# Kernel optimization log

Measured on AMD Instinct MI355X. Metric: run time of the kernel, lower is better.

## Reference

```python
import jax, jax.numpy as jnp
import numpy as np

B, T, S, G, D, H, W, CHUNK = 2, 4096, 4096, 64, 1024, 16, 512, 256
HD = D // H


def setup_inputs() -> dict:
    key = jax.random.key(0)
    ks = jax.random.split(key, 16)
    std = 1.0 / np.sqrt(D)
    w = lambda k: jax.random.normal(k, (D, D), jnp.float32) * std
    b = lambda k: jax.random.normal(k, (D,), jnp.float32) * 0.01
    return {
        "query": jax.random.normal(ks[0], (B, T, D), jnp.float32),
        "encoder_out": jax.random.normal(ks[1], (B, S, D), jnp.float32),
        "global_tokens": jax.random.normal(ks[2], (B, G, D), jnp.float32),
        "qw": w(ks[3]), "qb": b(ks[4]),
        "kw": w(ks[5]), "kb": b(ks[6]),
        "vw": w(ks[7]), "vb": b(ks[8]),
        "gkw": w(ks[9]), "gkb": b(ks[10]),
        "gvw": w(ks[11]), "gvb": b(ks[12]),
        "ow": w(ks[13]), "ob": b(ks[14]),
        "compression_ratio": 1,
    }


def reference(query, encoder_out, global_tokens, qw, qb, kw, kb, vw, vb,
              gkw, gkb, gvw, gvb, ow, ob, compression_ratio):
    scale = jnp.float32(np.sqrt(HD))
    r = jnp.float32(compression_ratio)
    # expected raw position for each decoder step, clamped to valid src range
    expected = jnp.clip((jnp.arange(T, dtype=jnp.float32) / r).astype(jnp.int32), 0, S - 1)
    expected = jnp.broadcast_to(expected[None], (B, T))  # [B,T]

    lin = lambda x, wt, bs: x @ wt.T + bs  # torch nn.Linear: y = x W^T + b
    q = lin(query, qw, qb).reshape(B, T, H, HD).transpose(0, 2, 1, 3)            # [B,H,T,HD]
    gk = lin(global_tokens, gkw, gkb).reshape(B, G, H, HD).transpose(0, 2, 1, 3)  # [B,H,G,HD]
    gv = lin(global_tokens, gvw, gvb).reshape(B, G, H, HD).transpose(0, 2, 1, 3)
    ak = lin(encoder_out, kw, kb).reshape(B, S, H, HD).transpose(0, 2, 1, 3)      # [B,H,S,HD]
    av = lin(encoder_out, vw, vb).reshape(B, S, H, HD).transpose(0, 2, 1, 3)

    nC = T // CHUNK
    # per-(batch,chunk) window start, from the middle query's expected position
    centers = expected.reshape(B, nC, CHUNK)[:, :, CHUNK // 2]   # [B,nC]
    win_start = jnp.clip(centers - W // 2, 0, S - W)             # [B,nC]; window always full length W
    idx = win_start[:, :, None] + jnp.arange(W)[None, None, :]   # [B,nC,W]

    gather = lambda kv_b, idx_b: kv_b[:, idx_b, :]               # [H,S,HD],[nC,W] -> [H,nC,W,HD]
    wk = jax.vmap(gather)(ak, idx)                               # [B,H,nC,W,HD]
    wv = jax.vmap(gather)(av, idx)

    qc = q.reshape(B, H, nC, CHUNK, HD)
    sg = jnp.einsum('bhcqd,bhgd->bhcqg', qc, gk) / scale          # global scores  [B,H,nC,CHUNK,G]
    sl = jnp.einsum('bhcqd,bhcwd->bhcqw', qc, wk) / scale         # windowed scores [B,H,nC,CHUNK,W]
    attn = jax.nn.softmax(jnp.concatenate([sg, sl], axis=-1), axis=-1)
    out = (jnp.einsum('bhcqg,bhgd->bhcqd', attn[..., :G], gv)
           + jnp.einsum('bhcqw,bhcwd->bhcqd', attn[..., G:], wv))  # [B,H,nC,CHUNK,HD]
    out = out.reshape(B, H, T, HD).transpose(0, 2, 1, 3).reshape(B, T, D)
    return lin(out, ow, ob)
```

## Files before the change

### kernel.cpp

```cpp
#include <hip/hip_runtime.h>

typedef unsigned short u16;
typedef unsigned int u32;
typedef __attribute__((ext_vector_type(4))) float f32x4;
typedef __attribute__((ext_vector_type(16))) float f32x16;
typedef __attribute__((ext_vector_type(8))) short bf16x8;

constexpr int B_ = 2, T_ = 4096, S_ = 4096, G_ = 64, D_ = 1024, H_ = 16, W_ = 512, CHUNK_ = 256;
constexpr int NC_ = T_ / CHUNK_;
constexpr int NT_ = (G_ + W_) / 32;

__device__ __forceinline__ u16 f2bf(float x) {
  u32 u = __builtin_bit_cast(u32, x);
  return (u16)((u + 0x7FFFu + ((u >> 16) & 1u)) >> 16);
}

__global__ __launch_bounds__(256) void cvt_all_kernel(const float* __restrict__ q, const float* __restrict__ e,
                                                      const float* __restrict__ g, const float* __restrict__ w0,
                                                      const float* __restrict__ w1, const float* __restrict__ w2,
                                                      const float* __restrict__ w3, const float* __restrict__ w4,
                                                      const float* __restrict__ w5, u16* __restrict__ dst) {
  int blk = blockIdx.x;
  const float* src;
  int sblk;
  if (blk < 8192) { src = q; sblk = 0; }
  else if (blk < 16384) { src = e; sblk = 8192; }
  else if (blk < 16512) { src = g; sblk = 16384; }
  else if (blk < 17536) { src = w0; sblk = 16512; }
  else if (blk < 18560) { src = w1; sblk = 17536; }
  else if (blk < 19584) { src = w2; sblk = 18560; }
  else if (blk < 20608) { src = w3; sblk = 19584; }
  else if (blk < 21632) { src = w4; sblk = 20608; }
  else { src = w5; sblk = 21632; }
  int li = (blk - sblk) * 256 + threadIdx.x;
  size_t gi = (size_t)blk * 256 + threadIdx.x;
  float4 v = ((const float4*)src)[li];
  uint2 o;
  o.x = (u32)f2bf(v.x) | ((u32)f2bf(v.y) << 16);
  o.y = (u32)f2bf(v.z) | ((u32)f2bf(v.w) << 16);
  ((uint2*)dst)[gi] = o;
}

template <int MODE>
__global__ __launch_bounds__(256) void gemm_kernel(const u16* __restrict__ A, const u16* __restrict__ Bt,
                                                   const float* __restrict__ bias, const float* __restrict__ bias2,
                                                   size_t split, void* __restrict__ out) {
  __shared__ char lds[32768];
  char* As = lds;
  char* Bs = lds + 16384;
  const int tid = threadIdx.x;
  const int lane = tid & 63;
  const int wv = tid >> 6;
  const int wr = wv >> 1, wc = wv & 1;
  const int l15 = lane & 15, kg = lane >> 4;
  const int row0 = blockIdx.x * 128;
  const int col0 = blockIdx.y * 128;

  f32x4 acc[4][4];
#pragma unroll
  for (int i = 0; i < 4; i++)
#pragma unroll
    for (int j = 0; j < 4; j++)
#pragma unroll
      for (int r = 0; r < 4; r++) acc[i][j][r] = 0.f;

  const char* Abase = (const char*)A;
  const char* Bbase = (const char*)Bt;

  const int kb = 16 * ((lane & 3) ^ ((lane >> 3) & 3));
  auto stage = [&](int bufsel, int k0) {
#pragma unroll
    for (int c = 0; c < 2; c++) {
      int arow = wv * 32 + c * 16 + (lane >> 2);
      int dsto = bufsel * 8192 + wv * 2048 + c * 1024 + lane * 16;
      const char* ga = Abase + ((size_t)(row0 + arow) * 2048 + (size_t)k0 * 2 + kb);
      __builtin_amdgcn_global_load_lds((const __attribute__((address_space(1))) void*)ga,
                                       (__attribute__((address_space(3))) void*)(As + dsto), 16, 0, 0);
      const char* gb = Bbase + ((size_t)(col0 + arow) * 2048 + (size_t)k0 * 2 + kb);
      __builtin_amdgcn_global_load_lds((const __attribute__((address_space(1))) void*)gb,
                                       (__attribute__((address_space(3))) void*)(Bs + dsto), 16, 0, 0);
    }
  };

  stage(0, 0);
  __syncthreads();

  for (int it = 0; it < 32; ++it) {
    const int cur = it & 1;
    if (it + 1 < 32) stage(cur ^ 1, (it + 1) * 32);

    const char* Ab = As + cur * 8192;
    const char* Bb = Bs + cur * 8192;
    bf16x8 af[4], bfv[4];
#pragma unroll
    for (int mi = 0; mi < 4; mi++) {
      int row = wr * 64 + mi * 16 + l15;
      af[mi] = *(const bf16x8*)(Ab + ((row * 64 + kg * 16) ^ ((row & 6) << 3)));
    }
#pragma unroll
    for (int ni = 0; ni < 4; ni++) {
      int row = wc * 64 + ni * 16 + l15;
      bfv[ni] = *(const bf16x8*)(Bb + ((row * 64 + kg * 16) ^ ((row & 6) << 3)));
    }
    __builtin_amdgcn_s_setprio(1);
#pragma unroll
    for (int mi = 0; mi < 4; mi++)
#pragma unroll
      for (int ni = 0; ni < 4; ni++)
        acc[mi][ni] = __builtin_amdgcn_mfma_f32_16x16x32_bf16(bfv[ni], af[mi], acc[mi][ni], 0, 0, 0);
    __builtin_amdgcn_s_setprio(0);
    __syncthreads();
  }

  const float* bp = bias;
  size_t obase = 0;
  if (MODE == 3 && col0 >= 1024) {
    bp = bias2 - 1024;
    obase = split - 1024;
  }
  float4 bv4[4];
#pragma unroll
  for (int ni = 0; ni < 4; ni++) bv4[ni] = *(const float4*)&bp[col0 + wc * 64 + ni * 16 + kg * 4];
#pragma unroll
  for (int mi = 0; mi < 4; mi++) {
    size_t grow = (size_t)(row0 + wr * 64 + mi * 16 + l15);
#pragma unroll
    for (int ni = 0; ni < 4; ni++) {
      int gcol = col0 + wc * 64 + ni * 16 + kg * 4;
      float v0 = acc[mi][ni][0] + bv4[ni].x;
      float v1 = acc[mi][ni][1] + bv4[ni].y;
      float v2 = acc[mi][ni][2] + bv4[ni].z;
      float v3 = acc[mi][ni][3] + bv4[ni].w;
      if (MODE == 1) {
        v0 *= 0.18033688011112042f; v1 *= 0.18033688011112042f;
        v2 *= 0.18033688011112042f; v3 *= 0.18033688011112042f;
      }
      if (MODE == 2) {
        float4 fo = {v0, v1, v2, v3};
        *(float4*)&((float*)out)[grow * 1024 + gcol] = fo;
      } else {
        uint2 o;
        asm("v_cvt_pk_bf16_f32 %0, %1, %2" : "=v"(o.x) : "v"(v0), "v"(v1));
        asm("v_cvt_pk_bf16_f32 %0, %1, %2" : "=v"(o.y) : "v"(v2), "v"(v3));
        *(uint2*)&((u16*)out)[obase + grow * 1024 + gcol] = o;
      }
    }
  }
}

__global__ __launch_bounds__(512, 4) void attn_kernel(const u16* __restrict__ q_bf, const u16* __restrict__ k_bf,
                                                      const u16* __restrict__ v_bf, const u16* __restrict__ gk_bf,
                                                      const u16* __restrict__ gv_bf, u16* __restrict__ ao,
                                                      const int* __restrict__ rptr) {
  __shared__ u16 smem[16384];
  const int c = blockIdx.x, h = blockIdx.y, b = blockIdx.z;
  const int tid = threadIdx.x;
  const int lane = tid & 63, wv = tid >> 6;
  const int l31 = lane & 31, half = lane >> 5;
  const int t0 = c * CHUNK_;

  int rr = rptr[0];
  int centert = c * CHUNK_ + CHUNK_ / 2;
  int expected = (int)((float)centert / (float)rr);
  expected = min(max(expected, 0), S_ - 1);
  int ws0 = min(max(expected - W_ / 2, 0), S_ - W_);

  bf16x8 qf[4];
  {
    const u16* qrow = q_bf + ((size_t)(b * T_ + t0 + wv * 32 + l31)) * D_ + h * 64 + half * 8;
#pragma unroll
    for (int s = 0; s < 4; s++) qf[s] = *(const bf16x8*)(qrow + s * 16);
  }

  const int skey = (tid & 255) >> 3, shq = tid & 7;
  const bool isK = tid < 256;

  auto load_tile = [&](int j) -> uint4 {
    const u16* base;
    size_t row;
    if (j < 2) {
      base = isK ? gk_bf : gv_bf;
      row = (size_t)(b * G_ + j * 32 + skey);
    } else {
      base = isK ? k_bf : v_bf;
      row = (size_t)(b * S_ + ws0 + (j - 2) * 32 + skey);
    }
    return *(const uint4*)(base + row * D_ + h * 64 + shq * 8);
  };

  f32x16 oacc[2];
#pragma unroll
  for (int i = 0; i < 2; i++)
#pragma unroll
    for (int r = 0; r < 16; r++) oacc[i][r] = 0.f;
  float mrun = -1e30f, lsum = 0.f;

  uint4 stg = load_tile(0);

  for (int j = 0; j < NT_; j++) {
    const int bsel = j & 1;
    if (isK) {
      *(uint4*)((char*)smem + bsel * 4096 + ((skey * 128 + shq * 16) ^ ((skey & 7) << 4))) = stg;
    } else {
      const u16* pv = (const u16*)&stg;
      char* bp = (char*)smem + 8192 + bsel * 5248 + shq * 656 + skey * 2;
#pragma unroll
      for (int e = 0; e < 8; e++) *(u16*)(bp + e * 80) = pv[e];
    }
    if (j + 1 < NT_) stg = load_tile(j + 1);
    __syncthreads();

    const int kbase = bsel * 4096;
    const int vtb = 8192 + bsel * 5248;

    f32x16 sacc;
#pragma unroll
    for (int r = 0; r < 16; r++) sacc[r] = 0.f;
    __builtin_amdgcn_s_setprio(1);
#pragma unroll
    for (int s = 0; s < 4; s++) {
      int kb = kbase + ((l31 * 128 + half * 16 + s * 32) ^ ((l31 & 7) << 4));
      bf16x8 kf = *(const bf16x8*)((char*)smem + kb);
      sacc = __builtin_amdgcn_mfma_f32_32x32x16_bf16(kf, qf[s], sacc, 0, 0, 0);
    }
    __builtin_amdgcn_s_setprio(0);

    float t0m = fmaxf(fmaxf(sacc[0], sacc[1]), sacc[2]);
    float t1m = fmaxf(fmaxf(sacc[3], sacc[4]), sacc[5]);
    float t2m = fmaxf(fmaxf(sacc[6], sacc[7]), sacc[8]);
    float t3m = fmaxf(fmaxf(sacc[9], sacc[10]), sacc[11]);
    float t4m = fmaxf(fmaxf(sacc[12], sacc[13]), sacc[14]);
    float tmax = fmaxf(fmaxf(fmaxf(t0m, t1m), fmaxf(t2m, t3m)), fmaxf(t4m, sacc[15]));
    tmax = fmaxf(tmax, __shfl_xor(tmax, 32));
    if (__any(tmax > mrun + 8.f)) {
      float mnew = fmaxf(mrun, tmax);
      float fac = __builtin_amdgcn_exp2f(mrun - mnew);
      mrun = mnew;
      lsum *= fac;
#pragma unroll
      for (int i = 0; i < 2; i++)
#pragma unroll
        for (int r = 0; r < 16; r++) oacc[i][r] *= fac;
    }
    float p[16];
#pragma unroll
    for (int r = 0; r < 16; r++) p[r] = __builtin_amdgcn_exp2f(sacc[r] - mrun);
    float s0s = (p[0] + p[1]) + (p[2] + p[3]);
    float s1s = (p[4] + p[5]) + (p[6] + p[7]);
    float s2s = (p[8] + p[9]) + (p[10] + p[11]);
    float s3s = (p[12] + p[13]) + (p[14] + p[15]);
    float tsum = (s0s + s1s) + (s2s + s3s);
    tsum += __shfl_xor(tsum, 32);
    lsum += tsum;

    u32 xs[8], px[8];
#pragma unroll
    for (int i = 0; i < 8; i++)
      asm("v_cvt_pk_bf16_f32 %0, %1, %2" : "=v"(xs[i]) : "v"(p[2 * i]), "v"(p[2 * i + 1]));
#pragma unroll
    for (int i = 0; i < 8; i++) px[i] = (u32)__shfl_xor((int)xs[i], 32);
    u32 Bk[2][4];
    Bk[0][0] = half ? px[2] : xs[0];
    Bk[0][1] = half ? px[3] : xs[1];
    Bk[0][2] = half ? xs[2] : px[0];
    Bk[0][3] = half ? xs[3] : px[1];
    Bk[1][0] = half ? px[6] : xs[4];
    Bk[1][1] = half ? px[7] : xs[5];
    Bk[1][2] = half ? xs[6] : px[4];
    Bk[1][3] = half ? xs[7] : px[5];

    int vro = vtb + l31 * 80 + ((l31 >> 3) << 4) + half * 16;
    __builtin_amdgcn_s_setprio(1);
#pragma unroll
    for (int hdf = 0; hdf < 2; hdf++) {
#pragma unroll
      for (int ks = 0; ks < 2; ks++) {
        bf16x8 vf = *(const bf16x8*)((const char*)smem + vro + hdf * 2624 + ks * 32);
        uint4 u4;
        u4.x = Bk[ks][0]; u4.y = Bk[ks][1]; u4.z = Bk[ks][2]; u4.w = Bk[ks][3];
        bf16x8 pb = __builtin_bit_cast(bf16x8, u4);
        oacc[hdf] = __builtin_amdgcn_mfma_f32_32x32x16_bf16(vf, pb, oacc[hdf], 0, 0, 0);
      }
    }
    __builtin_amdgcn_s_setprio(0);
  }

  __syncthreads();
  float inv = 1.f / lsum;
#pragma unroll
  for (int hdf = 0; hdf < 2; hdf++) {
#pragma unroll
    for (int a = 0; a < 4; a++) {
      float f0 = oacc[hdf][4 * a] * inv, f1 = oacc[hdf][4 * a + 1] * inv;
      float f2 = oacc[hdf][4 * a + 2] * inv, f3 = oacc[hdf][4 * a + 3] * inv;
      uint2 o;
      asm("v_cvt_pk_bf16_f32 %0, %1, %2" : "=v"(o.x) : "v"(f0), "v"(f1));
      asm("v_cvt_pk_bf16_f32 %0, %1, %2" : "=v"(o.y) : "v"(f2), "v"(f3));
      int off = wv * 4096 + l31 * 128 + ((16 * a + 8 * half + 64 * hdf) ^ ((l31 & 7) << 4));
      *(uint2*)((char*)smem + off) = o;
    }
  }
  __syncthreads();
#pragma unroll
  for (int it = 0; it < 4; it++) {
    int byteo = (tid + it * 512) * 16;
    int row = byteo >> 7;
    int colb = byteo & 127;
    uint4 vv = *(const uint4*)((const char*)smem + row * 128 + (colb ^ ((row & 7) << 4)));
    *(uint4*)(ao + ((size_t)(b * T_ + t0 + row)) * D_ + h * 64 + (colb >> 1)) = vv;
  }
}

extern "C" void kernel_launch(void* const* d_in, const int* in_sizes, int n_in,
                              void* d_out, int out_size, void* d_ws, size_t ws_size,
                              hipStream_t stream) {
  (void)in_sizes; (void)n_in; (void)out_size; (void)ws_size;
  const float* query = (const float*)d_in[0];
  const float* enc = (const float*)d_in[1];
  const float* glob = (const float*)d_in[2];
  const float* qw = (const float*)d_in[3];
  const float* qb = (const float*)d_in[4];
  const float* kw = (const float*)d_in[5];
  const float* kb = (const float*)d_in[6];
  const float* vw = (const float*)d_in[7];
  const float* vb = (const float*)d_in[8];
  const float* gkw = (const float*)d_in[9];
  const float* gkb = (const float*)d_in[10];
  const float* gvw = (const float*)d_in[11];
  const float* gvb = (const float*)d_in[12];
  const float* ow = (const float*)d_in[13];
  const float* ob = (const float*)d_in[14];
  const int* rp = (const int*)d_in[15];

  const size_t NQ = (size_t)B_ * T_ * D_;
  const size_t NG = (size_t)B_ * G_ * D_;
  const size_t NW = (size_t)D_ * D_;

  u16* ws = (u16*)d_ws;
  u16* qx = ws;
  u16* ex = qx + NQ;
  u16* gx = ex + NQ;
  u16* wgt = gx + NG;
  u16* q_bf = wgt + 6 * NW;
  u16* k_bf = q_bf + NQ;
  u16* v_bf = k_bf + NQ;
  u16* gk_bf = v_bf + NQ;
  u16* gv_bf = gk_bf + NG;
  u16* ao = gv_bf + NG;

  cvt_all_kernel<<<22656, 256, 0, stream>>>(query, enc, glob, qw, kw, vw, gkw, gvw, ow, ws);

  gemm_kernel<1><<<dim3(64, 8), 256, 0, stream>>>(qx, wgt + 0 * NW, qb, qb, 0, q_bf);
  gemm_kernel<3><<<dim3(64, 16), 256, 0, stream>>>(ex, wgt + 1 * NW, kb, vb, NQ, k_bf);
  gemm_kernel<3><<<dim3(1, 16), 256, 0, stream>>>(gx, wgt + 3 * NW, gkb, gvb, NG, gk_bf);

  attn_kernel<<<dim3(NC_, H_, B_), 512, 0, stream>>>(q_bf, k_bf, v_bf, gk_bf, gv_bf, ao, rp);

  gemm_kernel<2><<<dim3(64, 8), 256, 0, stream>>>(ao, wgt + 5 * NW, ob, ob, 0, d_out);
}
```

Measured before the change: 171.2 us.

## Use 256x256-tile triple-buffered GEMM kernel for fused K/V projection

Adds a new GEMM kernel that uses 256x256 output tiles with 512 threads. It stages tiles straight from global memory into LDS with global_load_lds, triple-buffers them, uses a swizzled LDS layout, and interleaves loads with MFMA phases. The fused K/V projection of encoder_out now uses this kernel instead of the generic one, aiming for more operand reuse per tile and better overlap of loads with compute. The grid becomes 256 blocks of 512 threads, which may fill the GPU's compute units less evenly, and the large 96 KB LDS footprint limits occupancy.

```diff
diff --git a/kernel.cpp b/kernel.cpp
--- a/kernel.cpp
+++ b/kernel.cpp
@@ -148,6 +148,136 @@
   }
 }
 
+template <int MODE>
+__global__ __launch_bounds__(512, 2) void gemm256_kernel(const u16* __restrict__ A, const u16* __restrict__ Bt,
+                                                         const float* __restrict__ bias, const float* __restrict__ bias2,
+                                                         size_t split, void* __restrict__ out) {
+  __shared__ char lds[98304];
+  const int tid = threadIdx.x;
+  const int lane = tid & 63;
+  const int wid = tid >> 6;
+  const int wm = wid >> 2, wn = wid & 3;
+  const int l15 = lane & 15, kg = lane >> 4;
+  const int bid = blockIdx.x;
+  const int swz = (bid & 7) * 32 + (bid >> 3);
+  const int row0 = (swz & 31) * 256;
+  const int col0 = (swz >> 5) * 256;
+
+  f32x4 acc[8][4];
+#pragma unroll
+  for (int i = 0; i < 8; i++)
+#pragma unroll
+    for (int j = 0; j < 4; j++)
+#pragma unroll
+      for (int r = 0; r < 4; r++) acc[i][j][r] = 0.f;
+
+  const char* Abase = (const char*)A;
+  const char* Bbase = (const char*)Bt;
+  const int kb = 16 * ((tid & 3) ^ ((tid >> 3) & 3));
+  const int rl0 = tid >> 2;
+
+  auto stageOp = [&](const char* base, int rowbase, int ldsbase, int kt) {
+#pragma unroll
+    for (int j = 0; j < 2; j++) {
+      int dst = ldsbase + tid * 16 + j * 8192;
+      const char* g = base + (size_t)(rowbase + rl0 + j * 128) * 2048 + kt * 64 + kb;
+      __builtin_amdgcn_global_load_lds((const __attribute__((address_space(1))) void*)g,
+                                       (__attribute__((address_space(3))) void*)(lds + dst), 16, 0, 0);
+    }
+  };
+
+  stageOp(Abase, row0, 0, 0);
+  stageOp(Bbase, col0, 49152, 0);
+  stageOp(Abase, row0, 16384, 1);
+  stageOp(Bbase, col0, 49152 + 16384, 1);
+  asm volatile("s_waitcnt vmcnt(4)" ::: "memory");
+  __builtin_amdgcn_s_barrier();
+
+  int cur = 0, nx = 2;
+  for (int t = 0; t < 32; ++t) {
+    const char* Ab = lds + cur * 16384;
+    const char* Bb = lds + 49152 + cur * 16384;
+    bf16x8 bfv[4], af[4];
+#pragma unroll
+    for (int ni = 0; ni < 4; ni++) {
+      int r = wn * 64 + ni * 16 + l15;
+      bfv[ni] = *(const bf16x8*)(Bb + ((r * 64 + kg * 16) ^ (((r >> 1) & 3) << 4)));
+    }
+#pragma unroll
+    for (int mi = 0; mi < 4; mi++) {
+      int r = wm * 128 + mi * 16 + l15;
+      af[mi] = *(const bf16x8*)(Ab + ((r * 64 + kg * 16) ^ (((r >> 1) & 3) << 4)));
+    }
+    if (t + 2 < 32) stageOp(Abase, row0, nx * 16384, t + 2);
+    __builtin_amdgcn_s_barrier();
+    __builtin_amdgcn_s_setprio(1);
+#pragma unroll
+    for (int mi = 0; mi < 4; mi++)
+#pragma unroll
+      for (int ni = 0; ni < 4; ni++)
+        acc[mi][ni] = __builtin_amdgcn_mfma_f32_16x16x32_bf16(bfv[ni], af[mi], acc[mi][ni], 0, 0, 0);
+    __builtin_amdgcn_s_setprio(0);
+    __builtin_amdgcn_s_barrier();
+#pragma unroll
+    for (int mi = 0; mi < 4; mi++) {
+      int r = wm * 128 + (mi + 4) * 16 + l15;
+      af[mi] = *(const bf16x8*)(Ab + ((r * 64 + kg * 16) ^ (((r >> 1) & 3) << 4)));
+    }
+    if (t + 2 < 32) stageOp(Bbase, col0, 49152 + nx * 16384, t + 2);
+    __builtin_amdgcn_s_barrier();
+    __builtin_amdgcn_s_setprio(1);
+#pragma unroll
+    for (int mi = 0; mi < 4; mi++)
+#pragma unroll
+      for (int ni = 0; ni < 4; ni++)
+        acc[mi + 4][ni] = __builtin_amdgcn_mfma_f32_16x16x32_bf16(bfv[ni], af[mi], acc[mi + 4][ni], 0, 0, 0);
+    __builtin_amdgcn_s_setprio(0);
+    if (t < 30) {
+      asm volatile("s_waitcnt vmcnt(4)" ::: "memory");
+    } else if (t == 30) {
+      asm volatile("s_waitcnt vmcnt(0)" ::: "memory");
+    }
+    __builtin_amdgcn_s_barrier();
+    cur = cur == 2 ? 0 : cur + 1;
+    nx = nx == 2 ? 0 : nx + 1;
+  }
+
+  const float* bp = bias;
+  size_t obase = 0;
+  if (MODE == 3 && col0 >= 1024) {
+    bp = bias2 - 1024;
+    obase = split - 1024;
+  }
+  float4 bv4[4];
+#pragma unroll
+  for (int ni = 0; ni < 4; ni++) bv4[ni] = *(const float4*)&bp[col0 + wn * 64 + ni * 16 + kg * 4];
+#pragma unroll
+  for (int mi = 0; mi < 8; mi++) {
+    size_t grow = (size_t)(row0 + wm * 128 + mi * 16 + l15);
+#pragma unroll
+    for (int ni = 0; ni < 4; ni++) {
+      int gcol = col0 + wn * 64 + ni * 16 + kg * 4;
+      float v0 = acc[mi][ni][0] + bv4[ni].x;
+      float v1 = acc[mi][ni][1] + bv4[ni].y;
+      float v2 = acc[mi][ni][2] + bv4[ni].z;
+      float v3 = acc[mi][ni][3] + bv4[ni].w;
+      if (MODE == 1) {
+        v0 *= 0.18033688011112042f; v1 *= 0.18033688011112042f;
+        v2 *= 0.18033688011112042f; v3 *= 0.18033688011112042f;
+      }
+      if (MODE == 2) {
+        float4 fo = {v0, v1, v2, v3};
+        *(float4*)&((float*)out)[grow * 1024 + gcol] = fo;
+      } else {
+        uint2 o;
+        asm("v_cvt_pk_bf16_f32 %0, %1, %2" : "=v"(o.x) : "v"(v0), "v"(v1));
+        asm("v_cvt_pk_bf16_f32 %0, %1, %2" : "=v"(o.y) : "v"(v2), "v"(v3));
+        *(uint2*)&((u16*)out)[obase + grow * 1024 + gcol] = o;
+      }
+    }
+  }
+}
+
 __global__ __launch_bounds__(512, 4) void attn_kernel(const u16* __restrict__ q_bf, const u16* __restrict__ k_bf,
                                                       const u16* __restrict__ v_bf, const u16* __restrict__ gk_bf,
                                                       const u16* __restrict__ gv_bf, u16* __restrict__ ao,
@@ -219,8 +349,8 @@
     __builtin_amdgcn_s_setprio(1);
 #pragma unroll
     for (int s = 0; s < 4; s++) {
-      int kb = kbase + ((l31 * 128 + half * 16 + s * 32) ^ ((l31 & 7) << 4));
-      bf16x8 kf = *(const bf16x8*)((char*)smem + kb);
+      int kbx = kbase + ((l31 * 128 + half * 16 + s * 32) ^ ((l31 & 7) << 4));
+      bf16x8 kf = *(const bf16x8*)((char*)smem + kbx);
       sacc = __builtin_amdgcn_mfma_f32_32x32x16_bf16(kf, qf[s], sacc, 0, 0, 0);
     }
     __builtin_amdgcn_s_setprio(0);
@@ -351,7 +481,7 @@
   cvt_all_kernel<<<22656, 256, 0, stream>>>(query, enc, glob, qw, kw, vw, gkw, gvw, ow, ws);
 
   gemm_kernel<1><<<dim3(64, 8), 256, 0, stream>>>(qx, wgt + 0 * NW, qb, qb, 0, q_bf);
-  gemm_kernel<3><<<dim3(64, 16), 256, 0, stream>>>(ex, wgt + 1 * NW, kb, vb, NQ, k_bf);
+  gemm256_kernel<3><<<256, 512, 0, stream>>>(ex, wgt + 1 * NW, kb, vb, NQ, k_bf);
   gemm_kernel<3><<<dim3(1, 16), 256, 0, stream>>>(gx, wgt + 3 * NW, gkb, gvb, NG, gk_bf);
 
   attn_kernel<<<dim3(NC_, H_, B_), 512, 0, stream>>>(q_bf, k_bf, v_bf, gk_bf, gv_bf, ao, rp);
```

Measured after the change: 164.2 us. 4.0% less time.
